# Kernel tuning notes

Hardware: AMD Instinct MI355X
Metric: run time of the kernel (lower is better)

Reference implementation:

```python
import jax, jax.numpy as jnp
import numpy as np
import math

B, S, H, DM = 1, 2048, 16, 1024
DK = DM // H
MAX_SEQ = 2048  # rel_embed has MAX_SEQ+1 rows


def setup_inputs() -> dict:
    rng = jax.random.key(0)
    ks = jax.random.split(rng, 12)
    w = lambda k, shape, s=0.02: (jax.random.normal(k, shape, jnp.float32) * s)
    inp = {
        'query': jax.random.normal(ks[0], (B, S, DM), jnp.float32),
        'key':   jax.random.normal(ks[1], (B, S, DM), jnp.float32),
        'value': jax.random.normal(ks[2], (B, S, DM), jnp.float32),
        # causal integer mask [B,S,S] (cumsum over it derives rel-pos indices)
        'mask': jnp.broadcast_to(jnp.tril(jnp.ones((S, S), jnp.int32)), (B, S, S)),
        'Wq': w(ks[3], (DM, DM)), 'bq': jnp.zeros((DM,), jnp.float32),
        'Wk': w(ks[4], (DM, DM)), 'bk': jnp.zeros((DM,), jnp.float32),
        'Wv': w(ks[5], (DM, DM)), 'bv': jnp.zeros((DM,), jnp.float32),
        'Wo': w(ks[6], (DM, DM)), 'bo': jnp.zeros((DM,), jnp.float32),
        # relative position embeddings [h, max_seq_len+1, d_k], N(0,1) as in the module
        'rel_embed': jax.random.normal(ks[7], (H, MAX_SEQ + 1, DK), jnp.float32),
    }
    return inp


def reference(query, key, value, mask, Wq, bq, Wk, bk, Wv, bv, Wo, bo, rel_embed):
    scale = 1.0 / math.sqrt(DK)
    heads = lambda x, W, b: (x @ W.T + b).reshape(B, S, H, DK).transpose(0, 2, 1, 3)
    q = heads(query, Wq, bq)   # [B,H,S,DK]
    k = heads(key, Wk, bk)
    v = heads(value, Wv, bv)

    scores = jnp.einsum('bhid,bhjd->bhij', q, k) * scale  # [B,H,S,S]

    m4 = mask[:, None, :, :]                 # [B,1,S,S]
    nz = m4 != 0
    # torch: cumsum(mask)-1 picks the m-index; index 0 (then zeroed) where mask==0
    m_idx = jnp.where(nz, jnp.cumsum(m4, axis=-1) - 1, 0)  # [B,1,S,S]

    # rel_scores[b,h,m,l] = <q[b,h,l,:], rel_embed[h,m,:]> / sqrt(d_k)
    rel = jnp.einsum('bhld,hmd->bhml', q, rel_embed[:, :S]) * scale  # [B,H,S,S]
    idx = jnp.broadcast_to(m_idx, (B, H, S, S))
    # torch.take flat-index decodes to rel[b,h, m_idx[i,j], j]
    rel_g = jnp.take_along_axis(rel, idx, axis=2) * nz.astype(scores.dtype)

    scores = jnp.where(nz, scores + rel_g, jnp.float32(-1e9))
    p = jax.nn.softmax(scores, axis=-1)      # dropout p=0.0 -> identity

    out = jnp.einsum('bhij,bhjd->bhid', p, v)         # [B,H,S,DK]
    out = out.transpose(0, 2, 1, 3).reshape(B, S, DM)  # [B,S,DM]
    return out @ Wo.T + bo
```

## Files before the change

kernel.cpp:

```cpp
#include <hip/hip_runtime.h>

typedef __bf16 bf16_t;
typedef __bf16 bf16x4 __attribute__((ext_vector_type(4)));
typedef __bf16 bf16x8 __attribute__((ext_vector_type(8)));
typedef float  f32x4  __attribute__((ext_vector_type(4)));
typedef float  f32x16 __attribute__((ext_vector_type(16)));
typedef unsigned int u32;

#define S_LEN 2048
#define DMODEL 1024
#define NHEAD 16
#define DHEAD 64
#define RELROWS 2049

__device__ __forceinline__ void gload16(const void* g, void* l) {
    __builtin_amdgcn_global_load_lds((const __attribute__((address_space(1))) void*)g,
                                     (__attribute__((address_space(3))) void*)l,
                                     16, 0, 0);
}

__device__ __forceinline__ f32x4 mfma16(bf16x8 a, bf16x8 b, f32x4 c) {
    return __builtin_amdgcn_mfma_f32_16x16x32_bf16(a, b, c, 0, 0, 0);
}
__device__ __forceinline__ f32x16 mfma32(bf16x8 a, bf16x8 b, f32x16 c) {
    return __builtin_amdgcn_mfma_f32_32x32x16_bf16(a, b, c, 0, 0, 0);
}

__device__ __forceinline__ bf16x8 lds_read_swz(const bf16_t* base, int row, int colb) {
    return *(const bf16x8*)((const char*)base + row * 128 + (colb ^ ((row & 7) << 4)));
}

__device__ __forceinline__ u32 cvtpk(float lo, float hi) {
    u32 w;
    asm("v_cvt_pk_bf16_f32 %0, %1, %2" : "=v"(w) : "v"(lo), "v"(hi));
    return w;
}
__device__ __forceinline__ void swap32(u32& a, u32& b) {
    asm("v_permlane32_swap_b32 %0, %1" : "+v"(a), "+v"(b));
}

__global__ __launch_bounds__(256)
void f2bf_all(const float* __restrict__ xq, const float* __restrict__ xk,
              const float* __restrict__ xv,
              const float* __restrict__ wq, const float* __restrict__ wk,
              const float* __restrict__ wv, const float* __restrict__ wo,
              bf16_t* __restrict__ dst, int n4X, int n4W) {
    const int i = blockIdx.x * blockDim.x + threadIdx.x;
    const float* src; int j;
    if (i < 3 * n4X) {
        if (i < n4X)            { src = xq; j = i; }
        else if (i < 2 * n4X)   { src = xk; j = i - n4X; }
        else                    { src = xv; j = i - 2 * n4X; }
    } else {
        int w = i - 3 * n4X;
        if (w < n4W)            { src = wq; j = w; }
        else if (w < 2 * n4W)   { src = wk; j = w - n4W; }
        else if (w < 3 * n4W)   { src = wv; j = w - 2 * n4W; }
        else                    { src = wo; j = w - 3 * n4W; }
    }
    float4 v = ((const float4*)src)[j];
    bf16x4 o;
    o[0] = (bf16_t)v.x; o[1] = (bf16_t)v.y; o[2] = (bf16_t)v.z; o[3] = (bf16_t)v.w;
    ((bf16x4*)dst)[i] = o;
}

template <int MODE, int BM, int BN>
__global__ __launch_bounds__(256)
void gemm_bt(const bf16_t* __restrict__ Abase, const bf16_t* __restrict__ Wbase,
             const float* __restrict__ b0, const float* __restrict__ b1,
             const float* __restrict__ b2,
             bf16_t* __restrict__ outb, float* __restrict__ outf,
             const float* __restrict__ relp, float* __restrict__ RGout,
             bf16_t* __restrict__ vtp,
             int M, int N, int K) {
    __shared__ alignas(16) bf16_t As[2][BM * 64];
    __shared__ alignas(16) bf16_t Bs[2][BN * 64];
    const int tid = threadIdx.x, lane = tid & 63, wave = tid >> 6;
    const int z = blockIdx.z;
    const bf16_t* A = Abase + (size_t)z * M * K;
    const bf16_t* W = Wbase + (size_t)z * N * K;
    const float* bias = (z == 0) ? b0 : (z == 1 ? b1 : b2);
    const int nwg = gridDim.x * gridDim.y;
    const int wg = blockIdx.y * gridDim.x + blockIdx.x;
    const int swz = (wg & 7) * (nwg >> 3) + (wg >> 3);
    const int m0 = (swz / gridDim.x) * BM, n0 = (swz % gridDim.x) * BN;
    const int wr = (wave >> 1) * (BM / 2), wc = (wave & 1) * (BN / 2);
    constexpr int MR = BM / 32, NR = BN / 32;
    constexpr int LOADS = BM / 32 + BN / 32;

    f32x4 acc[MR][NR] = {};
    const int soff = wave * 1024 + lane * 16;

    auto stage = [&](int b, int kt) {
#pragma unroll
        for (int r = 0; r < BM / 32; ++r) {
            int e = (r * 4096 + soff) >> 1;
            int row = e >> 6, col = e & 63;
            gload16(A + (size_t)(m0 + row) * K + kt + col,
                    (char*)As[b] + r * 4096 + wave * 1024);
        }
#pragma unroll
        for (int r = 0; r < BN / 32; ++r) {
            int e = (r * 4096 + soff) >> 1;
            int row = e >> 6, col = e & 63;
            gload16(W + (size_t)(n0 + row) * K + kt + col,
                    (char*)Bs[b] + r * 4096 + wave * 1024);
        }
    };

    const int NK = K >> 6;
    stage(0, 0);
    for (int s = 0; s < NK; ++s) {
        const int buf = s & 1;
        if (s + 1 < NK) {
            stage(buf ^ 1, (s + 1) << 6);
            if constexpr (LOADS == 6) asm volatile("s_waitcnt vmcnt(6)" ::: "memory");
            else if constexpr (LOADS == 4) asm volatile("s_waitcnt vmcnt(4)" ::: "memory");
            else asm volatile("s_waitcnt vmcnt(8)" ::: "memory");
        } else {
            asm volatile("s_waitcnt vmcnt(0)" ::: "memory");
        }
        asm volatile("s_barrier" ::: "memory");
#pragma unroll
        for (int kk = 0; kk < 2; ++kk) {
            bf16x8 af[MR], bfr[NR];
#pragma unroll
            for (int m = 0; m < MR; ++m)
                af[m] = *(const bf16x8*)&As[buf][(wr + m * 16 + (lane & 15)) * 64 + kk * 32 + (lane >> 4) * 8];
#pragma unroll
            for (int n = 0; n < NR; ++n)
                bfr[n] = *(const bf16x8*)&Bs[buf][(wc + n * 16 + (lane & 15)) * 64 + kk * 32 + (lane >> 4) * 8];
#pragma unroll
            for (int m = 0; m < MR; ++m)
#pragma unroll
                for (int n = 0; n < NR; ++n)
                    acc[m][n] = mfma16(af[m], bfr[n], acc[m][n]);
        }
        asm volatile("s_barrier" ::: "memory");
    }

    const float scale = (MODE == 0 && z == 0) ? 0.125f : 1.0f;
    float rp[MR][4];
    if constexpr (MODE == 0) {
#pragma unroll
        for (int m = 0; m < MR; ++m)
#pragma unroll
            for (int r2 = 0; r2 < 4; ++r2) rp[m][r2] = 0.f;
    }
    const int hh = n0 >> 6;
#pragma unroll
    for (int m = 0; m < MR; ++m) {
        const int gi = m0 + wr + m * 16 + (lane >> 4) * 4;
#pragma unroll
        for (int n = 0; n < NR; ++n) {
            const int gj = n0 + wc + n * 16 + (lane & 15);
            const float bv = bias[gj];
            if constexpr (MODE == 0) {
                if (z == 2) {
                    bf16x4 o4;
#pragma unroll
                    for (int r2 = 0; r2 < 4; ++r2) o4[r2] = (bf16_t)(acc[m][n][r2] + bv);
                    *(bf16x4*)&vtp[(size_t)gj * S_LEN + gi] = o4;
                } else {
#pragma unroll
                    for (int r2 = 0; r2 < 4; ++r2) {
                        float v = (acc[m][n][r2] + bv) * scale;
                        outb[(size_t)z * M * N + (size_t)(gi + r2) * N + gj] = (bf16_t)v;
                        if (z == 0)
                            rp[m][r2] += v * relp[((size_t)hh * RELROWS + (gi + r2)) * DHEAD + (gj & 63)];
                    }
                }
            } else {
#pragma unroll
                for (int r2 = 0; r2 < 4; ++r2)
                    outf[(size_t)(gi + r2) * N + gj] = acc[m][n][r2] + bv;
            }
        }
    }
    if constexpr (MODE == 0) {
        if (z == 0) {
            float* Rp = (float*)As;
#pragma unroll
            for (int m = 0; m < MR; ++m)
#pragma unroll
                for (int r2 = 0; r2 < 4; ++r2) {
                    float p = rp[m][r2];
                    p += __shfl_xor(p, 1);
                    p += __shfl_xor(p, 2);
                    p += __shfl_xor(p, 4);
                    p += __shfl_xor(p, 8);
                    if ((lane & 15) == 0)
                        Rp[wave * 64 + m * 16 + (lane >> 4) * 4 + r2] = p;
                }
            __syncthreads();
            if ((wave & 1) == 0) {
                float v = Rp[wave * 64 + lane] + Rp[(wave + 1) * 64 + lane];
                RGout[hh * S_LEN + m0 + wr + lane] = v;
            }
        }
    }
}

__global__ __launch_bounds__(256, 2)
void flash_attn(const bf16_t* __restrict__ Qb, const bf16_t* __restrict__ Kb,
                const bf16_t* __restrict__ Vtp, const float* __restrict__ RG,
                bf16_t* __restrict__ Ob) {
    __shared__ alignas(16) bf16_t KB[4][64 * 64];
    __shared__ alignas(16) bf16_t VB[4][64 * 64];
    __shared__ alignas(16) bf16_t Qs[64 * 64];
    __shared__ alignas(16) float Rs[S_LEN];
    const int tid = threadIdx.x, lane = tid & 63, wave = tid >> 6;
    const int qt = (int)gridDim.x - 1 - (int)blockIdx.x;
    const int h = blockIdx.y;
    const int q0 = qt * 64;
    const int nt = qt + 1;
    const int lo5 = lane & 31, hi = lane >> 5;
    const int qhalf = wave & 1;
    const int par = wave >> 1;

    const int nkv = nt * 64;
    if (tid * 8 < nkv) {
        float4 a = *(const float4*)&RG[h * S_LEN + tid * 8];
        float4 b = *(const float4*)&RG[h * S_LEN + tid * 8 + 4];
        *(float4*)&Rs[tid * 8] = a;
        *(float4*)&Rs[tid * 8 + 4] = b;
    }

    auto stage_tile = [&](int tt) {
        const int bse = tt & 3;
#pragma unroll
        for (int r2 = 0; r2 < 2; ++r2) {
            int rr = wave * 2 + r2;
            int L = rr * 1024 + lane * 16;
            int row = L >> 7, colb = (L & 127) ^ ((row & 7) << 4);
            gload16(Kb + (size_t)(tt * 64 + row) * DMODEL + h * DHEAD + (colb >> 1),
                    (char*)KB[bse] + rr * 1024);
            gload16(Vtp + (size_t)(h * DHEAD + row) * S_LEN + tt * 64 + (colb >> 1),
                    (char*)VB[bse] + rr * 1024);
        }
    };

#pragma unroll
    for (int r2 = 0; r2 < 2; ++r2) {
        int rr = wave * 2 + r2;
        int L = rr * 1024 + lane * 16;
        int row = L >> 7, colb = (L & 127) ^ ((row & 7) << 4);
        gload16(Qb + (size_t)(q0 + row) * DMODEL + h * DHEAD + (colb >> 1),
                (char*)Qs + rr * 1024);
    }
    stage_tile(0);
    stage_tile(nt > 1 ? 1 : 0);
    asm volatile("s_waitcnt vmcnt(8) lgkmcnt(0)\n\ts_barrier" ::: "memory");

    bf16x8 qf[4];
#pragma unroll
    for (int c = 0; c < 4; ++c)
        qf[c] = lds_read_swz(Qs, qhalf * 32 + lo5, c * 32 + hi * 16);

    f32x16 oacc[2] = {};
    float ls = 0.f;

    for (int t2 = 0; t2 < nt; t2 += 2) {
        if (t2 + 3 < nt) {
            stage_tile(t2 + 2);
            stage_tile(t2 + 3);
            asm volatile("s_waitcnt vmcnt(8)\n\ts_barrier" ::: "memory");
        } else if (t2 + 2 < nt) {
            stage_tile(t2 + 2);
            asm volatile("s_waitcnt vmcnt(4)\n\ts_barrier" ::: "memory");
        } else {
            asm volatile("s_waitcnt vmcnt(0)\n\ts_barrier" ::: "memory");
        }

        const int tt = t2 + par;
        if (tt < nt) {
            const int buf = tt & 3;
            const int kv0 = tt * 64;
            const bool diag = (tt == nt - 1);
            f32x16 sta, stb;
#pragma unroll
            for (int g = 0; g < 4; ++g) {
                f32x4 ra = *(const f32x4*)&Rs[kv0 + g * 8 + hi * 4];
                f32x4 rb = *(const f32x4*)&Rs[kv0 + 32 + g * 8 + hi * 4];
#pragma unroll
                for (int e = 0; e < 4; ++e) { sta[g * 4 + e] = ra[e]; stb[g * 4 + e] = rb[e]; }
            }
            __builtin_amdgcn_s_setprio(1);
#pragma unroll
            for (int c = 0; c < 4; ++c) {
                bf16x8 kfa = lds_read_swz(KB[buf], lo5, c * 32 + hi * 16);
                sta = mfma32(kfa, qf[c], sta);
            }
#pragma unroll
            for (int c = 0; c < 4; ++c) {
                bf16x8 kfb = lds_read_swz(KB[buf], 32 + lo5, c * 32 + hi * 16);
                stb = mfma32(kfb, qf[c], stb);
            }
            __builtin_amdgcn_s_setprio(0);
            float pra[16], prb[16];
            if (diag) {
#pragma unroll
                for (int r = 0; r < 16; ++r) {
                    int kloc = (r & 3) + 8 * (r >> 2) + 4 * hi;
                    float va = __expf(sta[r]), vb = __expf(stb[r]);
                    pra[r] = (kloc > qhalf * 32 + lo5) ? 0.f : va;
                    prb[r] = (kloc + 32 > qhalf * 32 + lo5) ? 0.f : vb;
                }
            } else {
#pragma unroll
                for (int r = 0; r < 16; ++r) { pra[r] = __expf(sta[r]); prb[r] = __expf(stb[r]); }
            }
#pragma unroll
            for (int r = 0; r < 16; ++r) ls += pra[r] + prb[r];
            u32 pw[4][4];
#pragma unroll
            for (int hf = 0; hf < 2; ++hf) {
                u32 a  = cvtpk(pra[8 * hf + 0], pra[8 * hf + 1]);
                u32 b  = cvtpk(pra[8 * hf + 4], pra[8 * hf + 5]);
                swap32(a, b);
                u32 c2 = cvtpk(pra[8 * hf + 2], pra[8 * hf + 3]);
                u32 d2 = cvtpk(pra[8 * hf + 6], pra[8 * hf + 7]);
                swap32(c2, d2);
                pw[hf][0] = a;  pw[hf][1] = c2;  pw[hf][2] = b;  pw[hf][3] = d2;
            }
#pragma unroll
            for (int hf = 0; hf < 2; ++hf) {
                u32 a  = cvtpk(prb[8 * hf + 0], prb[8 * hf + 1]);
                u32 b  = cvtpk(prb[8 * hf + 4], prb[8 * hf + 5]);
                swap32(a, b);
                u32 c2 = cvtpk(prb[8 * hf + 2], prb[8 * hf + 3]);
                u32 d2 = cvtpk(prb[8 * hf + 6], prb[8 * hf + 7]);
                swap32(c2, d2);
                pw[2 + hf][0] = a;  pw[2 + hf][1] = c2;  pw[2 + hf][2] = b;  pw[2 + hf][3] = d2;
            }
            __builtin_amdgcn_s_setprio(1);
#pragma unroll
            for (int kc = 0; kc < 4; ++kc) {
                union { u32 w[4]; bf16x8 v; } uu;
                uu.w[0] = pw[kc][0]; uu.w[1] = pw[kc][1]; uu.w[2] = pw[kc][2]; uu.w[3] = pw[kc][3];
#pragma unroll
                for (int db = 0; db < 2; ++db) {
                    bf16x8 vf = lds_read_swz(VB[buf], db * 32 + lo5, kc * 32 + hi * 16);
                    oacc[db] = mfma32(vf, uu.v, oacc[db]);
                }
            }
            __builtin_amdgcn_s_setprio(0);
        }
        asm volatile("s_barrier" ::: "memory");
    }

    asm volatile("s_waitcnt vmcnt(0)" ::: "memory");
    if (wave >= 2) {
        char* base = (char*)KB[0] + (wave - 2) * 9728 + lane * 144;
#pragma unroll
        for (int db = 0; db < 2; ++db)
#pragma unroll
            for (int g = 0; g < 4; ++g) {
                f32x4 v4;
#pragma unroll
                for (int e = 0; e < 4; ++e) v4[e] = oacc[db][g * 4 + e];
                *(f32x4*)(base + (db * 4 + g) * 16) = v4;
            }
        *(float*)((char*)KB[0] + 19456 + (wave - 2) * 256 + lane * 4) = ls;
    }
    __syncthreads();
    if (wave < 2) {
        const char* base = (const char*)KB[0] + wave * 9728 + lane * 144;
#pragma unroll
        for (int db = 0; db < 2; ++db)
#pragma unroll
            for (int g = 0; g < 4; ++g) {
                f32x4 v4 = *(const f32x4*)(base + (db * 4 + g) * 16);
#pragma unroll
                for (int e = 0; e < 4; ++e) oacc[db][g * 4 + e] += v4[e];
            }
        ls += *(const float*)((const char*)KB[0] + 19456 + wave * 256 + lane * 4);
        ls += __shfl_xor(ls, 32);
        const float inv = 1.0f / ls;
        const int qg = q0 + wave * 32 + lo5;
#pragma unroll
        for (int db = 0; db < 2; ++db)
#pragma unroll
            for (int g = 0; g < 4; ++g) {
                bf16x4 o4;
#pragma unroll
                for (int e = 0; e < 4; ++e)
                    o4[e] = (bf16_t)(oacc[db][g * 4 + e] * inv);
                *(bf16x4*)&Ob[(size_t)qg * DMODEL + h * DHEAD + db * 32 + g * 8 + hi * 4] = o4;
            }
    }
}

extern "C" void kernel_launch(void* const* d_in, const int* in_sizes, int n_in,
                              void* d_out, int out_size, void* d_ws, size_t ws_size,
                              hipStream_t stream) {
    const float* query = (const float*)d_in[0];
    const float* key   = (const float*)d_in[1];
    const float* value = (const float*)d_in[2];
    const float* Wq  = (const float*)d_in[4];
    const float* bq  = (const float*)d_in[5];
    const float* Wk  = (const float*)d_in[6];
    const float* bk  = (const float*)d_in[7];
    const float* Wv  = (const float*)d_in[8];
    const float* bv  = (const float*)d_in[9];
    const float* Wo  = (const float*)d_in[10];
    const float* bo  = (const float*)d_in[11];
    const float* rel = (const float*)d_in[12];

    char* ws = (char*)d_ws;
    const size_t nX = (size_t)S_LEN * DMODEL;
    const size_t nW = (size_t)DMODEL * DMODEL;
    bf16_t* Xbf  = (bf16_t*)ws;
    bf16_t* Wbf  = (bf16_t*)(ws + 3 * nX * 2);
    bf16_t* QKV  = (bf16_t*)(ws + 3 * nX * 2 + 4 * nW * 2);
    float*  RG   = (float*)(ws + 3 * nX * 2 + 4 * nW * 2 + 3 * nX * 2);
    bf16_t* Vtp  = QKV + 2 * nX;
    bf16_t* AOb  = (bf16_t*)(ws + nX * 2);
    (void)in_sizes; (void)n_in; (void)out_size; (void)ws_size;

    const int n4X = (int)(nX / 4), n4W = (int)(nW / 4);
    const int tot4 = 3 * n4X + 4 * n4W;
    f2bf_all<<<tot4 / 256, 256, 0, stream>>>(query, key, value, Wq, Wk, Wv, Wo,
                                             Xbf, n4X, n4W);

    gemm_bt<0, 128, 64><<<dim3(DMODEL / 64, S_LEN / 128, 3), 256, 0, stream>>>(
        Xbf, Wbf, bq, bk, bv, QKV, nullptr, rel, RG, Vtp, S_LEN, DMODEL, DMODEL);

    flash_attn<<<dim3(S_LEN / 64, NHEAD), 256, 0, stream>>>(QKV, QKV + nX, Vtp, RG, AOb);

    gemm_bt<1, 64, 64><<<dim3(DMODEL / 64, S_LEN / 64, 1), 256, 0, stream>>>(
        AOb, Wbf + 3 * nW, bo, bo, bo, nullptr, (float*)d_out,
        nullptr, nullptr, nullptr, S_LEN, DMODEL, DMODEL);
}
```

Before: 89.71 us.

## Load K/V fragments straight from global memory, dropping LDS staging in attention

The flash attention kernel stops staging Q, K and V tiles through a 4-deep LDS ring with async global-to-LDS loads and barriers. Each wave now reads its MFMA operand fragments directly from global memory, and the loop no longer has per-tile barriers. The grid is also transposed so consecutive blocks cover different heads of the same query tile. This removes LDS traffic and synchronisation and cuts LDS use, which may raise occupancy. The cost is uncoalesced 16-byte strided global loads with no software prefetch, and each K/V tile is read by two waves.

```diff
diff --git a/kernel.cpp b/kernel.cpp
--- a/kernel.cpp
+++ b/kernel.cpp
@@ -24,10 +24,6 @@
 }
 __device__ __forceinline__ f32x16 mfma32(bf16x8 a, bf16x8 b, f32x16 c) {
     return __builtin_amdgcn_mfma_f32_32x32x16_bf16(a, b, c, 0, 0, 0);
-}
-
-__device__ __forceinline__ bf16x8 lds_read_swz(const bf16_t* base, int row, int colb) {
-    return *(const bf16x8*)((const char*)base + row * 128 + (colb ^ ((row & 7) << 4)));
 }
 
 __device__ __forceinline__ u32 cvtpk(float lo, float hi) {
@@ -205,13 +201,11 @@
 void flash_attn(const bf16_t* __restrict__ Qb, const bf16_t* __restrict__ Kb,
                 const bf16_t* __restrict__ Vtp, const float* __restrict__ RG,
                 bf16_t* __restrict__ Ob) {
-    __shared__ alignas(16) bf16_t KB[4][64 * 64];
-    __shared__ alignas(16) bf16_t VB[4][64 * 64];
-    __shared__ alignas(16) bf16_t Qs[64 * 64];
     __shared__ alignas(16) float Rs[S_LEN];
+    __shared__ alignas(16) float Comb[2][2112];
     const int tid = threadIdx.x, lane = tid & 63, wave = tid >> 6;
-    const int qt = (int)gridDim.x - 1 - (int)blockIdx.x;
-    const int h = blockIdx.y;
+    const int h = blockIdx.x;
+    const int qt = (int)gridDim.y - 1 - (int)blockIdx.y;
     const int q0 = qt * 64;
     const int nt = qt + 1;
     const int lo5 = lane & 31, hi = lane >> 5;
@@ -219,139 +213,101 @@
     const int par = wave >> 1;
 
     const int nkv = nt * 64;
-    if (tid * 8 < nkv) {
-        float4 a = *(const float4*)&RG[h * S_LEN + tid * 8];
-        float4 b = *(const float4*)&RG[h * S_LEN + tid * 8 + 4];
-        *(float4*)&Rs[tid * 8] = a;
-        *(float4*)&Rs[tid * 8 + 4] = b;
-    }
-
-    auto stage_tile = [&](int tt) {
-        const int bse = tt & 3;
-#pragma unroll
-        for (int r2 = 0; r2 < 2; ++r2) {
-            int rr = wave * 2 + r2;
-            int L = rr * 1024 + lane * 16;
-            int row = L >> 7, colb = (L & 127) ^ ((row & 7) << 4);
-            gload16(Kb + (size_t)(tt * 64 + row) * DMODEL + h * DHEAD + (colb >> 1),
-                    (char*)KB[bse] + rr * 1024);
-            gload16(Vtp + (size_t)(h * DHEAD + row) * S_LEN + tt * 64 + (colb >> 1),
-                    (char*)VB[bse] + rr * 1024);
-        }
-    };
-
-#pragma unroll
-    for (int r2 = 0; r2 < 2; ++r2) {
-        int rr = wave * 2 + r2;
-        int L = rr * 1024 + lane * 16;
-        int row = L >> 7, colb = (L & 127) ^ ((row & 7) << 4);
-        gload16(Qb + (size_t)(q0 + row) * DMODEL + h * DHEAD + (colb >> 1),
-                (char*)Qs + rr * 1024);
-    }
-    stage_tile(0);
-    stage_tile(nt > 1 ? 1 : 0);
-    asm volatile("s_waitcnt vmcnt(8) lgkmcnt(0)\n\ts_barrier" ::: "memory");
-
+    for (int i = tid * 8; i < nkv; i += 2048) {
+        *(float4*)&Rs[i]     = *(const float4*)&RG[h * S_LEN + i];
+        *(float4*)&Rs[i + 4] = *(const float4*)&RG[h * S_LEN + i + 4];
+    }
+    __syncthreads();
+
+    const bf16_t* qp = Qb + (size_t)(q0 + qhalf * 32 + lo5) * DMODEL + h * DHEAD;
     bf16x8 qf[4];
 #pragma unroll
     for (int c = 0; c < 4; ++c)
-        qf[c] = lds_read_swz(Qs, qhalf * 32 + lo5, c * 32 + hi * 16);
+        qf[c] = *(const bf16x8*)(qp + c * 16 + hi * 8);
+
+    const bf16_t* Kh = Kb + h * DHEAD;
+    const bf16_t* Vh = Vtp + (size_t)h * DHEAD * S_LEN;
 
     f32x16 oacc[2] = {};
     float ls = 0.f;
 
-    for (int t2 = 0; t2 < nt; t2 += 2) {
-        if (t2 + 3 < nt) {
-            stage_tile(t2 + 2);
-            stage_tile(t2 + 3);
-            asm volatile("s_waitcnt vmcnt(8)\n\ts_barrier" ::: "memory");
-        } else if (t2 + 2 < nt) {
-            stage_tile(t2 + 2);
-            asm volatile("s_waitcnt vmcnt(4)\n\ts_barrier" ::: "memory");
+    for (int tt = par; tt < nt; tt += 2) {
+        const int kv0 = tt * 64;
+        const bool diag = (tt == nt - 1);
+        bf16x8 kfa[4], kfb[4];
+#pragma unroll
+        for (int c = 0; c < 4; ++c) {
+            kfa[c] = *(const bf16x8*)(Kh + (size_t)(kv0 + lo5) * DMODEL + c * 16 + hi * 8);
+            kfb[c] = *(const bf16x8*)(Kh + (size_t)(kv0 + 32 + lo5) * DMODEL + c * 16 + hi * 8);
+        }
+        f32x16 sta, stb;
+#pragma unroll
+        for (int g = 0; g < 4; ++g) {
+            f32x4 ra = *(const f32x4*)&Rs[kv0 + g * 8 + hi * 4];
+            f32x4 rb = *(const f32x4*)&Rs[kv0 + 32 + g * 8 + hi * 4];
+#pragma unroll
+            for (int e = 0; e < 4; ++e) { sta[g * 4 + e] = ra[e]; stb[g * 4 + e] = rb[e]; }
+        }
+        __builtin_amdgcn_s_setprio(1);
+#pragma unroll
+        for (int c = 0; c < 4; ++c) sta = mfma32(kfa[c], qf[c], sta);
+#pragma unroll
+        for (int c = 0; c < 4; ++c) stb = mfma32(kfb[c], qf[c], stb);
+        __builtin_amdgcn_s_setprio(0);
+
+        float pra[16], prb[16];
+        if (diag) {
+#pragma unroll
+            for (int r = 0; r < 16; ++r) {
+                int kloc = (r & 3) + 8 * (r >> 2) + 4 * hi;
+                float va = __expf(sta[r]), vb = __expf(stb[r]);
+                pra[r] = (kloc > qhalf * 32 + lo5) ? 0.f : va;
+                prb[r] = (kloc + 32 > qhalf * 32 + lo5) ? 0.f : vb;
+            }
         } else {
-            asm volatile("s_waitcnt vmcnt(0)\n\ts_barrier" ::: "memory");
-        }
-
-        const int tt = t2 + par;
-        if (tt < nt) {
-            const int buf = tt & 3;
-            const int kv0 = tt * 64;
-            const bool diag = (tt == nt - 1);
-            f32x16 sta, stb;
-#pragma unroll
-            for (int g = 0; g < 4; ++g) {
-                f32x4 ra = *(const f32x4*)&Rs[kv0 + g * 8 + hi * 4];
-                f32x4 rb = *(const f32x4*)&Rs[kv0 + 32 + g * 8 + hi * 4];
-#pragma unroll
-                for (int e = 0; e < 4; ++e) { sta[g * 4 + e] = ra[e]; stb[g * 4 + e] = rb[e]; }
-            }
-            __builtin_amdgcn_s_setprio(1);
-#pragma unroll
-            for (int c = 0; c < 4; ++c) {
-                bf16x8 kfa = lds_read_swz(KB[buf], lo5, c * 32 + hi * 16);
-                sta = mfma32(kfa, qf[c], sta);
-            }
-#pragma unroll
-            for (int c = 0; c < 4; ++c) {
-                bf16x8 kfb = lds_read_swz(KB[buf], 32 + lo5, c * 32 + hi * 16);
-                stb = mfma32(kfb, qf[c], stb);
-            }
-            __builtin_amdgcn_s_setprio(0);
-            float pra[16], prb[16];
-            if (diag) {
-#pragma unroll
-                for (int r = 0; r < 16; ++r) {
-                    int kloc = (r & 3) + 8 * (r >> 2) + 4 * hi;
-                    float va = __expf(sta[r]), vb = __expf(stb[r]);
-                    pra[r] = (kloc > qhalf * 32 + lo5) ? 0.f : va;
-                    prb[r] = (kloc + 32 > qhalf * 32 + lo5) ? 0.f : vb;
-                }
-            } else {
-#pragma unroll
-                for (int r = 0; r < 16; ++r) { pra[r] = __expf(sta[r]); prb[r] = __expf(stb[r]); }
-            }
-#pragma unroll
-            for (int r = 0; r < 16; ++r) ls += pra[r] + prb[r];
-            u32 pw[4][4];
-#pragma unroll
-            for (int hf = 0; hf < 2; ++hf) {
-                u32 a  = cvtpk(pra[8 * hf + 0], pra[8 * hf + 1]);
-                u32 b  = cvtpk(pra[8 * hf + 4], pra[8 * hf + 5]);
-                swap32(a, b);
-                u32 c2 = cvtpk(pra[8 * hf + 2], pra[8 * hf + 3]);
-                u32 d2 = cvtpk(pra[8 * hf + 6], pra[8 * hf + 7]);
-                swap32(c2, d2);
-                pw[hf][0] = a;  pw[hf][1] = c2;  pw[hf][2] = b;  pw[hf][3] = d2;
-            }
-#pragma unroll
-            for (int hf = 0; hf < 2; ++hf) {
-                u32 a  = cvtpk(prb[8 * hf + 0], prb[8 * hf + 1]);
-                u32 b  = cvtpk(prb[8 * hf + 4], prb[8 * hf + 5]);
-                swap32(a, b);
-                u32 c2 = cvtpk(prb[8 * hf + 2], prb[8 * hf + 3]);
-                u32 d2 = cvtpk(prb[8 * hf + 6], prb[8 * hf + 7]);
-                swap32(c2, d2);
-                pw[2 + hf][0] = a;  pw[2 + hf][1] = c2;  pw[2 + hf][2] = b;  pw[2 + hf][3] = d2;
-            }
-            __builtin_amdgcn_s_setprio(1);
-#pragma unroll
-            for (int kc = 0; kc < 4; ++kc) {
-                union { u32 w[4]; bf16x8 v; } uu;
-                uu.w[0] = pw[kc][0]; uu.w[1] = pw[kc][1]; uu.w[2] = pw[kc][2]; uu.w[3] = pw[kc][3];
-#pragma unroll
-                for (int db = 0; db < 2; ++db) {
-                    bf16x8 vf = lds_read_swz(VB[buf], db * 32 + lo5, kc * 32 + hi * 16);
-                    oacc[db] = mfma32(vf, uu.v, oacc[db]);
-                }
-            }
-            __builtin_amdgcn_s_setprio(0);
-        }
-        asm volatile("s_barrier" ::: "memory");
-    }
-
-    asm volatile("s_waitcnt vmcnt(0)" ::: "memory");
+#pragma unroll
+            for (int r = 0; r < 16; ++r) { pra[r] = __expf(sta[r]); prb[r] = __expf(stb[r]); }
+        }
+#pragma unroll
+        for (int r = 0; r < 16; ++r) ls += pra[r] + prb[r];
+        u32 pw[4][4];
+#pragma unroll
+        for (int hf = 0; hf < 2; ++hf) {
+            u32 a  = cvtpk(pra[8 * hf + 0], pra[8 * hf + 1]);
+            u32 b  = cvtpk(pra[8 * hf + 4], pra[8 * hf + 5]);
+            swap32(a, b);
+            u32 c2 = cvtpk(pra[8 * hf + 2], pra[8 * hf + 3]);
+            u32 d2 = cvtpk(pra[8 * hf + 6], pra[8 * hf + 7]);
+            swap32(c2, d2);
+            pw[hf][0] = a;  pw[hf][1] = c2;  pw[hf][2] = b;  pw[hf][3] = d2;
+        }
+#pragma unroll
+        for (int hf = 0; hf < 2; ++hf) {
+            u32 a  = cvtpk(prb[8 * hf + 0], prb[8 * hf + 1]);
+            u32 b  = cvtpk(prb[8 * hf + 4], prb[8 * hf + 5]);
+            swap32(a, b);
+            u32 c2 = cvtpk(prb[8 * hf + 2], prb[8 * hf + 3]);
+            u32 d2 = cvtpk(prb[8 * hf + 6], prb[8 * hf + 7]);
+            swap32(c2, d2);
+            pw[2 + hf][0] = a;  pw[2 + hf][1] = c2;  pw[2 + hf][2] = b;  pw[2 + hf][3] = d2;
+        }
+        __builtin_amdgcn_s_setprio(1);
+#pragma unroll
+        for (int kc = 0; kc < 4; ++kc) {
+            union { u32 w[4]; bf16x8 v; } uu;
+            uu.w[0] = pw[kc][0]; uu.w[1] = pw[kc][1]; uu.w[2] = pw[kc][2]; uu.w[3] = pw[kc][3];
+#pragma unroll
+            for (int db = 0; db < 2; ++db) {
+                bf16x8 vf = *(const bf16x8*)(Vh + (size_t)(db * 32 + lo5) * S_LEN
+                                             + kv0 + kc * 16 + hi * 8);
+                oacc[db] = mfma32(vf, uu.v, oacc[db]);
+            }
+        }
+        __builtin_amdgcn_s_setprio(0);
+    }
+
     if (wave >= 2) {
-        char* base = (char*)KB[0] + (wave - 2) * 9728 + lane * 144;
+        float* base = &Comb[wave - 2][lane * 32];
 #pragma unroll
         for (int db = 0; db < 2; ++db)
 #pragma unroll
@@ -359,22 +315,22 @@
                 f32x4 v4;
 #pragma unroll
                 for (int e = 0; e < 4; ++e) v4[e] = oacc[db][g * 4 + e];
-                *(f32x4*)(base + (db * 4 + g) * 16) = v4;
-            }
-        *(float*)((char*)KB[0] + 19456 + (wave - 2) * 256 + lane * 4) = ls;
+                *(f32x4*)(base + db * 16 + g * 4) = v4;
+            }
+        Comb[wave - 2][2048 + lane] = ls;
     }
     __syncthreads();
     if (wave < 2) {
-        const char* base = (const char*)KB[0] + wave * 9728 + lane * 144;
+        const float* base = &Comb[wave][lane * 32];
 #pragma unroll
         for (int db = 0; db < 2; ++db)
 #pragma unroll
             for (int g = 0; g < 4; ++g) {
-                f32x4 v4 = *(const f32x4*)(base + (db * 4 + g) * 16);
+                f32x4 v4 = *(const f32x4*)(base + db * 16 + g * 4);
 #pragma unroll
                 for (int e = 0; e < 4; ++e) oacc[db][g * 4 + e] += v4[e];
             }
-        ls += *(const float*)((const char*)KB[0] + 19456 + wave * 256 + lane * 4);
+        ls += Comb[wave][2048 + lane];
         ls += __shfl_xor(ls, 32);
         const float inv = 1.0f / ls;
         const int qg = q0 + wave * 32 + lo5;
@@ -426,7 +382,7 @@
     gemm_bt<0, 128, 64><<<dim3(DMODEL / 64, S_LEN / 128, 3), 256, 0, stream>>>(
         Xbf, Wbf, bq, bk, bv, QKV, nullptr, rel, RG, Vtp, S_LEN, DMODEL, DMODEL);
 
-    flash_attn<<<dim3(S_LEN / 64, NHEAD), 256, 0, stream>>>(QKV, QKV + nX, Vtp, RG, AOb);
+    flash_attn<<<dim3(NHEAD, S_LEN / 64), 256, 0, stream>>>(QKV, QKV + nX, Vtp, RG, AOb);
 
     gemm_bt<1, 64, 64><<<dim3(DMODEL / 64, S_LEN / 64, 1), 256, 0, stream>>>(
         AOb, Wbf + 3 * nW, bo, bo, bo, nullptr, (float*)d_out,
```

New measurement: 107.0 us. 19.3% more time.
